# Performance work log

Hardware: AMD Instinct MI355X
Metric: run time of the kernel (lower is better)

## Reference

```python
import jax, jax.numpy as jnp
import numpy as np

EPS = 1e-8
NEG_FILL = -9e15


def _normalize(x):
    # matches torch cosine_similarity's norm clamp with eps=1e-8
    n = jnp.sqrt(jnp.sum(x * x, axis=-1, keepdims=True))
    return x / jnp.maximum(n, EPS)


def setup_inputs() -> dict:
    key = jax.random.key(0)
    k1, k2 = jax.random.split(key)
    N, D = 8192, 512
    cxr_feats = jax.random.normal(k1, (N, D), dtype=jnp.float32)
    ehr_feats = jax.random.normal(k2, (N, D), dtype=jnp.float32)
    temperature = jnp.asarray(0.07, dtype=jnp.float32)
    return {"cxr_feats": cxr_feats, "ehr_feats": ehr_feats, "temperature": temperature}


def reference(cxr_feats, ehr_feats, temperature):
    # normalize then GEMM instead of broadcasted [N,N,D] cosine_similarity
    cn = _normalize(cxr_feats)                      # [N, D]
    en = _normalize(ehr_feats)                      # [N, D]
    cos_sim = jnp.einsum('id,jd->ij', cn, en)       # [N, N]
    cos_sim = cos_sim / temperature
    N = cos_sim.shape[0]
    eye = jnp.eye(N, dtype=bool)
    diag = jnp.diagonal(cos_sim)                    # positives
    cos_neg = jnp.where(eye, NEG_FILL, cos_sim)     # mask self-pairs
    nll_1 = diag - jax.nn.logsumexp(cos_neg, axis=1)
    nll_2 = diag - jax.nn.logsumexp(cos_neg, axis=0)
    loss = -jnp.mean(nll_1 + nll_2)
    return loss
```

## Files before the change

kernel.cpp:

```cpp
#include <hip/hip_runtime.h>
#include <hip/hip_bf16.h>
#include <stdint.h>
#include <stddef.h>

#define NROWS 8192
#define DDIM  512
#define TILE  128
#define BKB   128
#define NBLK  (NROWS / TILE)

static_assert(NBLK == 64, "bj extraction assumes 64 col-blocks");

typedef float f32x4 __attribute__((ext_vector_type(4)));
typedef long  v2l  __attribute__((ext_vector_type(2)));

__device__ __forceinline__ void async_copy16(const void* g, void* l) {
    __builtin_amdgcn_global_load_lds(
        (const __attribute__((address_space(1))) uint32_t*)g,
        (__attribute__((address_space(3))) uint32_t*)l,
        16, 0, 0);
}

__global__ __launch_bounds__(256) void prep_kernel(
    const float* __restrict__ CXR, const float* __restrict__ EHR,
    uint32_t* __restrict__ CN8, uint32_t* __restrict__ EN8,
    float* __restrict__ rowsum ,
    float* __restrict__ out)
{
    if (blockIdx.x < 64) {
        rowsum[blockIdx.x * 256 + threadIdx.x] = 0.f;
        if (blockIdx.x == 0 && threadIdx.x == 0) out[0] = 0.f;
    }
    const int half = (blockIdx.x >= 2048);
    const float* X = half ? EHR : CXR;
    uint32_t* Y = half ? EN8 : CN8;
    const int row  = (blockIdx.x & 2047) * 4 + (threadIdx.x >> 6);
    const int lane = threadIdx.x & 63;
    const float* xr = X + (size_t)row * DDIM;
    float4 v0 = ((const float4*)xr)[lane];
    float4 v1 = ((const float4*)xr)[lane + 64];
    float ss = v0.x*v0.x + v0.y*v0.y + v0.z*v0.z + v0.w*v0.w
             + v1.x*v1.x + v1.y*v1.y + v1.z*v1.z + v1.w*v1.w;
    #pragma unroll
    for (int d = 1; d < 64; d <<= 1) ss += __shfl_xor(ss, d);
    const float sc = 1.0f / fmaxf(sqrtf(ss), 1e-8f);
    uint32_t* yr = Y + (size_t)row * (DDIM / 4);
    int w0 = __builtin_amdgcn_cvt_pk_fp8_f32(v0.x*sc, v0.y*sc, 0, false);
    w0     = __builtin_amdgcn_cvt_pk_fp8_f32(v0.z*sc, v0.w*sc, w0, true);
    int w1 = __builtin_amdgcn_cvt_pk_fp8_f32(v1.x*sc, v1.y*sc, 0, false);
    w1     = __builtin_amdgcn_cvt_pk_fp8_f32(v1.z*sc, v1.w*sc, w1, true);
    yr[lane]      = (uint32_t)w0;
    yr[lane + 64] = (uint32_t)w1;
}

__global__ __launch_bounds__(256, 2) void gemm_loss_kernel(
    const uint8_t* __restrict__ A,
    const uint8_t* __restrict__ B,
    const float* __restrict__ temp_p,
    float* __restrict__ rowsum,
    float* __restrict__ colsum,
    float* __restrict__ diagv)
{
    __shared__ uint8_t As[TILE * BKB];
    __shared__ uint8_t Bs[TILE * BKB];

    const int tid  = threadIdx.x;
    const int lane = tid & 63;
    const int wv   = tid >> 6;
    const int wi   = (wv >> 1) * 64;
    const int wj   = (wv & 1) * 64;
    const int lcol = lane & 15;
    const int q    = lane >> 4;

    const int bi = blockIdx.x & (NBLK - 1);
    const int bj = blockIdx.x >> 6;
    const int row0 = bi * TILE;
    const int col0 = bj * TILE;

    const int sr = lane >> 3;
    const int su = (lane & 7) ^ sr;
    const uint8_t* Ag = A + (size_t)(row0 + wv * 32 + sr) * DDIM + su * 16;
    const uint8_t* Bg = B + (size_t)(col0 + wv * 32 + sr) * DDIM + su * 16;

    f32x4 acc[4][4] = {};

    for (int k0 = 0; k0 < DDIM; k0 += BKB) {
        __syncthreads();
        #pragma unroll
        for (int c = 0; c < 4; ++c) {
            async_copy16(Ag + (size_t)(c * 8) * DDIM + k0, &As[(wv * 32 + c * 8) * BKB]);
            async_copy16(Bg + (size_t)(c * 8) * DDIM + k0, &Bs[(wv * 32 + c * 8) * BKB]);
        }
        __syncthreads();

        #pragma unroll
        for (int kk2 = 0; kk2 < 2; ++kk2) {
            const int u = kk2 * 4 + q;
            long aflo[4], afhi[4];
            #pragma unroll
            for (int mt = 0; mt < 4; ++mt) {
                const int r = wi + mt * 16 + lcol;
                v2l a16 = *(const v2l*)&As[r * BKB + (u ^ (r & 7)) * 16];
                aflo[mt] = a16.x; afhi[mt] = a16.y;
            }
            #pragma unroll
            for (int nt = 0; nt < 4; ++nt) {
                const int r = wj + nt * 16 + lcol;
                v2l b16 = *(const v2l*)&Bs[r * BKB + (u ^ (r & 7)) * 16];
                #pragma unroll
                for (int mt = 0; mt < 4; ++mt)
                    acc[mt][nt] = __builtin_amdgcn_mfma_f32_16x16x32_fp8_fp8(
                        aflo[mt], b16.x, acc[mt][nt], 0, 0, 0);
                #pragma unroll
                for (int mt = 0; mt < 4; ++mt)
                    acc[mt][nt] = __builtin_amdgcn_mfma_f32_16x16x32_fp8_fp8(
                        afhi[mt], b16.y, acc[mt][nt], 0, 0, 0);
            }
        }
    }

    const float invT = 1.0f / temp_p[0];
    const float M = invT;

    float rs[4][4];
    float cs[4];
    #pragma unroll
    for (int mt = 0; mt < 4; ++mt)
        #pragma unroll
        for (int r = 0; r < 4; ++r) rs[mt][r] = 0.f;
    #pragma unroll
    for (int nt = 0; nt < 4; ++nt) cs[nt] = 0.f;

    #pragma unroll
    for (int mt = 0; mt < 4; ++mt) {
        #pragma unroll
        for (int nt = 0; nt < 4; ++nt) {
            #pragma unroll
            for (int r = 0; r < 4; ++r) {
                const int gi = row0 + wi + mt * 16 + q * 4 + r;
                const int gj = col0 + wj + nt * 16 + lcol;
                const float sv = acc[mt][nt][r] * invT;
                float e;
                if (gi == gj) { diagv[gi] = sv; e = 0.f; }
                else          { e = __expf(sv - M); }
                rs[mt][r] += e;
                cs[nt]    += e;
            }
        }
    }

    #pragma unroll
    for (int d = 1; d < 16; d <<= 1)
        #pragma unroll
        for (int mt = 0; mt < 4; ++mt)
            #pragma unroll
            for (int r = 0; r < 4; ++r)
                rs[mt][r] += __shfl_xor(rs[mt][r], d);

    #pragma unroll
    for (int d = 16; d < 64; d <<= 1)
        #pragma unroll
        for (int nt = 0; nt < 4; ++nt)
            cs[nt] += __shfl_xor(cs[nt], d);

    if (lcol == 0) {
        #pragma unroll
        for (int mt = 0; mt < 4; ++mt)
            #pragma unroll
            for (int r = 0; r < 4; ++r)
                atomicAdd(&rowsum[row0 + wi + mt * 16 + q * 4 + r], rs[mt][r]);
    }
    if (q == 0) {
        #pragma unroll
        for (int nt = 0; nt < 4; ++nt)
            atomicAdd(&colsum[col0 + wj + nt * 16 + lcol], cs[nt]);
    }
}

__global__ __launch_bounds__(256) void finalize_kernel(
    const float* __restrict__ rowsum, const float* __restrict__ colsum,
    const float* __restrict__ diagv,  const float* __restrict__ temp_p,
    float* __restrict__ out)
{
    __shared__ float red[4];
    const float M = 1.0f / temp_p[0];
    const int i = blockIdx.x * 256 + threadIdx.x;
    float s = 2.f * M + logf(rowsum[i]) + logf(colsum[i]) - 2.f * diagv[i];
    #pragma unroll
    for (int d = 1; d < 64; d <<= 1) s += __shfl_xor(s, d);
    if ((threadIdx.x & 63) == 0) red[threadIdx.x >> 6] = s;
    __syncthreads();
    if (threadIdx.x == 0)
        atomicAdd(out, (red[0] + red[1] + red[2] + red[3]) / (float)NROWS);
}

extern "C" void kernel_launch(void* const* d_in, const int* in_sizes, int n_in,
                              void* d_out, int out_size, void* d_ws, size_t ws_size,
                              hipStream_t stream) {
    (void)in_sizes; (void)n_in; (void)out_size; (void)ws_size;
    const float* cxr    = (const float*)d_in[0];
    const float* ehr    = (const float*)d_in[1];
    const float* temp_p = (const float*)d_in[2];
    float* out = (float*)d_out;

    float* rowsum = (float*)d_ws;
    float* colsum = rowsum + NROWS;
    float* diagv  = colsum + NROWS;
    uint32_t* cn8 = (uint32_t*)(diagv + NROWS);
    uint32_t* en8 = cn8 + (size_t)NROWS * (DDIM / 4);
    const uint8_t* cnb = (const uint8_t*)cn8;
    const uint8_t* enb = (const uint8_t*)en8;

    prep_kernel<<<4096, 256, 0, stream>>>(cxr, ehr, cn8, en8, rowsum, out);
    gemm_loss_kernel<<<NBLK * NBLK, 256, 0, stream>>>(cnb, enb, temp_p, rowsum, colsum, diagv);
    finalize_kernel<<<NROWS / 256, 256, 0, stream>>>(rowsum, colsum, diagv, temp_p, out);
}
```

Before: 136.7 us.

## Double-buffer LDS K-stages with async prefetch and vmcnt-based waits

Splits the shared A/B tiles into two buffers and issues the global-to-LDS copies for the next K-stage before computing on the current one. Explicit vmcnt/lgkmcnt waits and raw barriers replace the two __syncthreads per iteration, and the K loop is fully unrolled. The aim is to hide global load latency behind the MFMA work. In exchange it doubles LDS use to 64KB per block, which may limit occupancy under launch_bounds(256,2), and the hand-written waitcnt sequencing is fragile.

```diff
diff --git a/kernel.cpp b/kernel.cpp
--- a/kernel.cpp
+++ b/kernel.cpp
@@ -61,8 +61,8 @@
     float* __restrict__ colsum,
     float* __restrict__ diagv)
 {
-    __shared__ uint8_t As[TILE * BKB];
-    __shared__ uint8_t Bs[TILE * BKB];
+    __shared__ uint8_t As[2][TILE * BKB];
+    __shared__ uint8_t Bs[2][TILE * BKB];
 
     const int tid  = threadIdx.x;
     const int lane = tid & 63;
@@ -77,22 +77,33 @@
     const int row0 = bi * TILE;
     const int col0 = bj * TILE;
 
+    const float invT = 1.0f / temp_p[0];
+    const float M = invT;
+
     const int sr = lane >> 3;
     const int su = (lane & 7) ^ sr;
     const uint8_t* Ag = A + (size_t)(row0 + wv * 32 + sr) * DDIM + su * 16;
     const uint8_t* Bg = B + (size_t)(col0 + wv * 32 + sr) * DDIM + su * 16;
 
+    auto stage_dma = [&](int s, int b) {
+        const int k0 = s * BKB;
+        #pragma unroll
+        for (int c = 0; c < 4; ++c) {
+            async_copy16(Ag + (size_t)(c * 8) * DDIM + k0, &As[b][(wv * 32 + c * 8) * BKB]);
+            async_copy16(Bg + (size_t)(c * 8) * DDIM + k0, &Bs[b][(wv * 32 + c * 8) * BKB]);
+        }
+    };
+
     f32x4 acc[4][4] = {};
 
-    for (int k0 = 0; k0 < DDIM; k0 += BKB) {
-        __syncthreads();
-        #pragma unroll
-        for (int c = 0; c < 4; ++c) {
-            async_copy16(Ag + (size_t)(c * 8) * DDIM + k0, &As[(wv * 32 + c * 8) * BKB]);
-            async_copy16(Bg + (size_t)(c * 8) * DDIM + k0, &Bs[(wv * 32 + c * 8) * BKB]);
-        }
-        __syncthreads();
-
+    stage_dma(0, 0);
+    stage_dma(1, 1);
+    asm volatile("s_waitcnt vmcnt(8)" ::: "memory");
+    __builtin_amdgcn_s_barrier();
+
+    #pragma unroll
+    for (int s = 0; s < 4; ++s) {
+        const int cur = s & 1;
         #pragma unroll
         for (int kk2 = 0; kk2 < 2; ++kk2) {
             const int u = kk2 * 4 + q;
@@ -100,13 +111,13 @@
             #pragma unroll
             for (int mt = 0; mt < 4; ++mt) {
                 const int r = wi + mt * 16 + lcol;
-                v2l a16 = *(const v2l*)&As[r * BKB + (u ^ (r & 7)) * 16];
+                v2l a16 = *(const v2l*)&As[cur][r * BKB + (u ^ (r & 7)) * 16];
                 aflo[mt] = a16.x; afhi[mt] = a16.y;
             }
             #pragma unroll
             for (int nt = 0; nt < 4; ++nt) {
                 const int r = wj + nt * 16 + lcol;
-                v2l b16 = *(const v2l*)&Bs[r * BKB + (u ^ (r & 7)) * 16];
+                v2l b16 = *(const v2l*)&Bs[cur][r * BKB + (u ^ (r & 7)) * 16];
                 #pragma unroll
                 for (int mt = 0; mt < 4; ++mt)
                     acc[mt][nt] = __builtin_amdgcn_mfma_f32_16x16x32_fp8_fp8(
@@ -117,10 +128,17 @@
                         afhi[mt], b16.y, acc[mt][nt], 0, 0, 0);
             }
         }
-    }
-
-    const float invT = 1.0f / temp_p[0];
-    const float M = invT;
+        if (s < 2) {
+            asm volatile("s_waitcnt lgkmcnt(0)" ::: "memory");
+            __builtin_amdgcn_s_barrier();
+            stage_dma(s + 2, cur);
+            asm volatile("s_waitcnt vmcnt(8)" ::: "memory");
+            __builtin_amdgcn_s_barrier();
+        } else if (s == 2) {
+            asm volatile("s_waitcnt vmcnt(0)" ::: "memory");
+            __builtin_amdgcn_s_barrier();
+        }
+    }
 
     float rs[4][4];
     float cs[4];
```

New measurement: 158.8 us. +16.1%, slower.
